# Optimization experiments

Hardware: AMD Instinct MI355X
Metric: run time of the kernel (lower is better)

Reference implementation:

```python
import jax, jax.numpy as jnp
import numpy as np
from jax import lax

ALPHA = 0.1
B, C_IN, T, D_MODEL = 32, 512, 2048, 1024


def setup_inputs() -> dict:
    key = jax.random.key(0)
    k_x, k_w, k_b = jax.random.split(key, 3)
    x = jax.random.normal(k_x, (B, C_IN, T), dtype=jnp.float32)
    # nn.Linear(c_in, d_model): weight [d_model, c_in], bias [d_model]
    bound = 1.0 / np.sqrt(C_IN)
    W = jax.random.uniform(k_w, (D_MODEL, C_IN), dtype=jnp.float32, minval=-bound, maxval=bound)
    b = jax.random.uniform(k_b, (D_MODEL,), dtype=jnp.float32, minval=-bound, maxval=bound)
    return {"x": x, "W": W, "b": b}


def _ewma_scan(xt):
    # xt: [T, B, C] time-major; f_0 = x_0, f_t = a*x_t + (1-a)*f_{t-1}
    def step(carry, xi):
        carry = ALPHA * xi + (1.0 - ALPHA) * carry
        return carry, carry
    _, ys = lax.scan(step, xt[0], xt[1:])
    return jnp.concatenate([xt[:1], ys], axis=0)  # [T, B, C]


def reference(x, W, b):
    # x: [B, c_in, T] -> permute to [B, T, c_in]
    xp = jnp.transpose(x, (0, 2, 1))
    xt = jnp.moveaxis(xp, 1, 0)  # [T, B, c_in]
    fwd = _ewma_scan(xt)
    bwd = _ewma_scan(xt[::-1])[::-1]
    ewma = jnp.moveaxis((fwd + bwd) * 0.5, 0, 1)  # [B, T, c_in]
    # value embedding (dropout = identity at inference)
    return jnp.einsum('btc,dc->btd', ewma, W) + b
```

## Files before the change

### kernel.cpp

```cpp
#include <hip/hip_runtime.h>
#include <hip/hip_bf16.h>
#include <stdint.h>
#include <stddef.h>

#define T_LEN   2048
#define C_IN_   512
#define D_MODEL_ 1024
#define B_SZ    32

typedef __hip_bfloat16 bf16;
typedef __attribute__((ext_vector_type(8))) short short8;
typedef __attribute__((ext_vector_type(4))) float f32x4;

__device__ __forceinline__ void gload16(const void* g, void* l) {
    __builtin_amdgcn_global_load_lds(
        (const __attribute__((address_space(1))) uint32_t*)g,
        (__attribute__((address_space(3))) uint32_t*)l, 16, 0, 0);
}

__global__ void wconv_kernel(const float* __restrict__ W, bf16* __restrict__ Wb) {
    int i = blockIdx.x * 256 + threadIdx.x;
    float4 v = ((const float4*)W)[i];
    bf16* o = Wb + (size_t)i * 4;
    o[0] = __float2bfloat16(v.x);
    o[1] = __float2bfloat16(v.y);
    o[2] = __float2bfloat16(v.z);
    o[3] = __float2bfloat16(v.w);
}

__global__ __launch_bounds__(512)
void ewma_kernel(const float* __restrict__ x, bf16* __restrict__ A) {
    const int tid  = threadIdx.x;
    const int wid  = tid >> 6;
    const int lane = tid & 63;
    const int half = lane >> 5;
    const int j    = lane & 31;
    const int b    = blockIdx.x >> 5;
    const int cg   = blockIdx.x & 31;
    const int c_local = (wid << 1) | half;
    const int c    = (cg << 4) + c_local;

    const float AL = 0.1f, OM = 0.9f;
    const float Q  = 1.179018457773862e-3f;

    float xr[64];
    const float4* xp = (const float4*)(x + (size_t)(b * C_IN_ + c) * T_LEN + j * 64);
    #pragma unroll
    for (int i = 0; i < 16; ++i) {
        float4 v = xp[i];
        xr[4*i+0] = v.x; xr[4*i+1] = v.y; xr[4*i+2] = v.z; xr[4*i+3] = v.w;
    }

    float g = (j == 0) ? xr[0] : AL * xr[0];
    #pragma unroll
    for (int i = 1; i < 64; ++i) g = fmaf(OM, g, AL * xr[i]);

    float F = g, coef = Q;
    #pragma unroll
    for (int d = 1; d < 32; d <<= 1) {
        float up = __shfl_up(F, d, 32);
        F += (j >= d) ? coef * up : 0.0f;
        coef *= coef;
    }
    float carry = __shfl_up(F, 1, 32);
    if (j == 0) carry = 0.0f;

    xr[0] = (j == 0) ? xr[0] : fmaf(OM, carry, AL * xr[0]);
    #pragma unroll
    for (int i = 1; i < 64; ++i) xr[i] = fmaf(OM, xr[i-1], AL * xr[i]);

    float h;
    {
        float incL = xr[63] - OM * xr[62];
        if (j == 31) incL *= 10.0f;
        h = incL;
        #pragma unroll
        for (int i = 62; i >= 1; --i) h = fmaf(OM, h, xr[i] - OM * xr[i-1]);
        float inc0 = (j == 0) ? AL * xr[0] : (xr[0] - OM * carry);
        h = fmaf(OM, h, inc0);
    }

    float Bv = h; coef = Q;
    #pragma unroll
    for (int d = 1; d < 32; d <<= 1) {
        float dn = __shfl_down(Bv, d, 32);
        Bv += (j < 32 - d) ? coef * dn : 0.0f;
        coef *= coef;
    }
    float bnext = __shfl_down(Bv, 1, 32);
    if (j == 31) bnext = 0.0f;

    {
        float bp = bnext;
        float incL = xr[63] - OM * xr[62];
        if (j == 31) incL *= 10.0f;
        float bb = fmaf(OM, bp, incL);
        xr[63] = 0.5f * (xr[63] + bb);
        bp = bb;
        #pragma unroll
        for (int i = 62; i >= 1; --i) {
            float inc = xr[i] - OM * xr[i-1];
            bb = fmaf(OM, bp, inc);
            xr[i] = 0.5f * (xr[i] + bb);
            bp = bb;
        }
        float inc0 = (j == 0) ? AL * xr[0] : (xr[0] - OM * carry);
        bb = fmaf(OM, bp, inc0);
        xr[0] = 0.5f * (xr[0] + bb);
    }

    __shared__ bf16 stg[32 * 16 * 16];
    const size_t outbase = (size_t)(b * T_LEN) * C_IN_ + (cg << 4);
    #pragma unroll
    for (int grp = 0; grp < 4; ++grp) {
        __syncthreads();
        #pragma unroll
        for (int ii = 0; ii < 16; ++ii) {
            int elem = ((j * 16 + ii) * 16 + c_local) ^ ((j & 7) << 3);
            stg[elem] = __float2bfloat16(xr[grp * 16 + ii]);
        }
        __syncthreads();
        #pragma unroll
        for (int r = 0; r < 2; ++r) {
            int u   = tid * 2 + r;
            int jj  = u >> 5;
            int ii  = (u >> 1) & 15;
            int hf  = u & 1;
            int elem = ((jj * 16 + ii) * 16 + hf * 8) ^ ((jj & 7) << 3);
            float4 v = *(const float4*)&stg[elem];
            int t = jj * 64 + grp * 16 + ii;
            *(float4*)(A + outbase + (size_t)t * C_IN_ + hf * 8) = v;
        }
    }
}

__global__ __launch_bounds__(256)
void gemm_kernel(const bf16* __restrict__ Amat, const bf16* __restrict__ Wb,
                 const float* __restrict__ bias, float* __restrict__ out) {
    constexpr int K = C_IN_, N = D_MODEL_, BK = 64;
    __shared__ bf16 As[128 * BK];
    __shared__ bf16 Bs[128 * BK];
    const int tid = threadIdx.x;
    const int wid = tid >> 6, lane = tid & 63;
    const int nb = blockIdx.x & 7, mb = blockIdx.x >> 3;
    const int m0 = mb * 128, n0 = nb * 128;
    const int wr = wid >> 1, wc = wid & 1;
    const int lrow = lane & 15, lk = (lane >> 4) * 8;

    f32x4 acc[4][4];
    #pragma unroll
    for (int i = 0; i < 4; ++i)
        #pragma unroll
        for (int q = 0; q < 4; ++q) acc[i][q] = (f32x4){0.f, 0.f, 0.f, 0.f};

    for (int kt = 0; kt < K; kt += BK) {
        const char* Ag = (const char*)(Amat + (size_t)m0 * K + kt);
        const char* Bg = (const char*)(Wb   + (size_t)n0 * K + kt);
        #pragma unroll
        for (int r = 0; r < 4; ++r) {
            int fb  = r * 4096 + tid * 16;
            int row = fb >> 7;
            int kb  = fb & 127;
            gload16(Ag + (size_t)row * (K * 2) + kb, (char*)As + fb);
            gload16(Bg + (size_t)row * (K * 2) + kb, (char*)Bs + fb);
        }
        __syncthreads();
        #pragma unroll
        for (int ks = 0; ks < 2; ++ks) {
            short8 af[4], bff[4];
            #pragma unroll
            for (int mf = 0; mf < 4; ++mf)
                af[mf] = *(const short8*)&As[(wr * 64 + mf * 16 + lrow) * BK + ks * 32 + lk];
            #pragma unroll
            for (int nf = 0; nf < 4; ++nf)
                bff[nf] = *(const short8*)&Bs[(wc * 64 + nf * 16 + lrow) * BK + ks * 32 + lk];
            #pragma unroll
            for (int mf = 0; mf < 4; ++mf)
                #pragma unroll
                for (int nf = 0; nf < 4; ++nf)
                    acc[mf][nf] = __builtin_amdgcn_mfma_f32_16x16x32_bf16(
                        af[mf], bff[nf], acc[mf][nf], 0, 0, 0);
        }
        __syncthreads();
    }
    #pragma unroll
    for (int mf = 0; mf < 4; ++mf) {
        #pragma unroll
        for (int nf = 0; nf < 4; ++nf) {
            int mrow0 = m0 + wr * 64 + mf * 16 + (lane >> 4) * 4;
            int ncol  = n0 + wc * 64 + nf * 16 + (lane & 15);
            float bv = bias[ncol];
            #pragma unroll
            for (int r = 0; r < 4; ++r)
                out[(size_t)(mrow0 + r) * N + ncol] = acc[mf][nf][r] + bv;
        }
    }
}

extern "C" void kernel_launch(void* const* d_in, const int* in_sizes, int n_in,
                              void* d_out, int out_size, void* d_ws, size_t ws_size,
                              hipStream_t stream) {
    const float* x    = (const float*)d_in[0];
    const float* W    = (const float*)d_in[1];
    const float* bias = (const float*)d_in[2];
    float* out = (float*)d_out;

    bf16* Wb   = (bf16*)d_ws;
    bf16* Amat = (bf16*)((char*)d_ws + (1 << 21));

    hipLaunchKernelGGL(wconv_kernel, dim3(512), dim3(256), 0, stream, W, Wb);
    hipLaunchKernelGGL(ewma_kernel, dim3(B_SZ * 32), dim3(512), 0, stream, x, Amat);
    hipLaunchKernelGGL(gemm_kernel, dim3((B_SZ * T_LEN / 128) * (D_MODEL_ / 128)),
                       dim3(256), 0, stream, Amat, Wb, bias, out);
}
```

Before: 204.7 us.

## Rewrite GEMM with 256x256 tiles, 8 waves, double-buffered swizzled LDS pipeline

Replaces the 128x128, 4-wave GEMM with a 256x256 tile computed by 512 threads using 128KB dynamic LDS. Global-to-LDS loads are double-buffered across K steps and interleaved with MFMA quadrants, using setprio and barriers. LDS rows are XOR-swizzled to avoid bank conflicts, and the block index is remapped for L2 locality. This raises data reuse and overlaps loads with compute, at the cost of LDS-limited occupancy of one block per CU and complex wait-count logic.

Result: faster. 172.6 us (-15.7%).

```diff
diff --git a/kernel.cpp b/kernel.cpp
--- a/kernel.cpp
+++ b/kernel.cpp
@@ -134,65 +134,148 @@
     }
 }
 
-__global__ __launch_bounds__(256)
+#define MFMA(a, b, c) __builtin_amdgcn_mfma_f32_16x16x32_bf16(a, b, c, 0, 0, 0)
+
+__global__ __launch_bounds__(512)
 void gemm_kernel(const bf16* __restrict__ Amat, const bf16* __restrict__ Wb,
                  const float* __restrict__ bias, float* __restrict__ out) {
-    constexpr int K = C_IN_, N = D_MODEL_, BK = 64;
-    __shared__ bf16 As[128 * BK];
-    __shared__ bf16 Bs[128 * BK];
-    const int tid = threadIdx.x;
-    const int wid = tid >> 6, lane = tid & 63;
-    const int nb = blockIdx.x & 7, mb = blockIdx.x >> 3;
-    const int m0 = mb * 128, n0 = nb * 128;
-    const int wr = wid >> 1, wc = wid & 1;
-    const int lrow = lane & 15, lk = (lane >> 4) * 8;
-
-    f32x4 acc[4][4];
-    #pragma unroll
-    for (int i = 0; i < 4; ++i)
-        #pragma unroll
-        for (int q = 0; q < 4; ++q) acc[i][q] = (f32x4){0.f, 0.f, 0.f, 0.f};
-
-    for (int kt = 0; kt < K; kt += BK) {
-        const char* Ag = (const char*)(Amat + (size_t)m0 * K + kt);
-        const char* Bg = (const char*)(Wb   + (size_t)n0 * K + kt);
-        #pragma unroll
-        for (int r = 0; r < 4; ++r) {
-            int fb  = r * 4096 + tid * 16;
-            int row = fb >> 7;
-            int kb  = fb & 127;
-            gload16(Ag + (size_t)row * (K * 2) + kb, (char*)As + fb);
-            gload16(Bg + (size_t)row * (K * 2) + kb, (char*)Bs + fb);
-        }
-        __syncthreads();
-        #pragma unroll
-        for (int ks = 0; ks < 2; ++ks) {
-            short8 af[4], bff[4];
-            #pragma unroll
-            for (int mf = 0; mf < 4; ++mf)
-                af[mf] = *(const short8*)&As[(wr * 64 + mf * 16 + lrow) * BK + ks * 32 + lk];
-            #pragma unroll
-            for (int nf = 0; nf < 4; ++nf)
-                bff[nf] = *(const short8*)&Bs[(wc * 64 + nf * 16 + lrow) * BK + ks * 32 + lk];
-            #pragma unroll
-            for (int mf = 0; mf < 4; ++mf)
-                #pragma unroll
-                for (int nf = 0; nf < 4; ++nf)
-                    acc[mf][nf] = __builtin_amdgcn_mfma_f32_16x16x32_bf16(
-                        af[mf], bff[nf], acc[mf][nf], 0, 0, 0);
-        }
-        __syncthreads();
-    }
-    #pragma unroll
-    for (int mf = 0; mf < 4; ++mf) {
-        #pragma unroll
-        for (int nf = 0; nf < 4; ++nf) {
-            int mrow0 = m0 + wr * 64 + mf * 16 + (lane >> 4) * 4;
-            int ncol  = n0 + wc * 64 + nf * 16 + (lane & 15);
-            float bv = bias[ncol];
+    constexpr int K = C_IN_, N = D_MODEL_;
+    extern __shared__ bf16 lds[];
+    const int tid  = threadIdx.x;
+    const int wid  = tid >> 6, lane = tid & 63;
+    const int wr   = wid >> 2, wc = wid & 3;
+    const int lr   = lane & 15;
+    const int lg   = lane >> 4;
+
+    int bid = blockIdx.x;
+    int swz = (bid & 7) * 128 + (bid >> 3);
+    const int mb = swz >> 2, nb = swz & 3;
+    const int m0 = mb * 256, n0 = nb * 256;
+
+    auto base = [&](int s, int op, int hf) -> bf16* {
+        return lds + (((s * 2 + op) * 2 + hf) << 13);
+    };
+    auto stage = [&](const bf16* g, int row0, int kt, int s, int op, int hf) {
+        bf16* lb = base(s, op, hf);
+        #pragma unroll
+        for (int r = 0; r < 2; ++r) {
+            int q = tid + r * 512;
+            int row = q >> 3, u = q & 7;
+            gload16(g + (size_t)(row0 + row) * K + kt * 64 + ((u ^ (row & 7)) << 3),
+                    (char*)lb + q * 16);
+        }
+    };
+    auto rdA = [&](int s, int mf, int ks) -> short8 {
+        int row = mf * 16 + lr;
+        int u   = ks * 4 + lg;
+        return *(const short8*)((const char*)base(s, 0, wr)
+                                + row * 128 + ((u ^ (row & 7)) << 4));
+    };
+    auto rdB = [&](int s, int nf, int ks) -> short8 {
+        int row = (wc & 1) * 64 + nf * 16 + lr;
+        int u   = ks * 4 + lg;
+        return *(const short8*)((const char*)base(s, 1, wc >> 1)
+                                + row * 128 + ((u ^ (row & 7)) << 4));
+    };
+
+    f32x4 acc[8][4];
+    #pragma unroll
+    for (int m = 0; m < 8; ++m)
+        #pragma unroll
+        for (int n = 0; n < 4; ++n) acc[m][n] = (f32x4){0.f, 0.f, 0.f, 0.f};
+
+    stage(Amat, m0 + 0,   0, 0, 0, 0);
+    stage(Amat, m0 + 128, 0, 0, 0, 1);
+    stage(Wb,   n0 + 0,   0, 0, 1, 0);
+    stage(Wb,   n0 + 128, 0, 0, 1, 1);
+    stage(Amat, m0 + 0,   1, 1, 0, 0);
+    asm volatile("s_waitcnt vmcnt(2)" ::: "memory");
+    __builtin_amdgcn_s_barrier();
+
+    #pragma unroll
+    for (int kt = 0; kt < 8; ++kt) {
+        const int s = kt & 1;
+        short8 a[4][2], bA[2][2], bB[2][2];
+
+        #pragma unroll
+        for (int m = 0; m < 4; ++m) { a[m][0] = rdA(s, m, 0); a[m][1] = rdA(s, m, 1); }
+        #pragma unroll
+        for (int n = 0; n < 2; ++n) { bA[n][0] = rdB(s, n, 0); bA[n][1] = rdB(s, n, 1); }
+        if (kt < 7) stage(Amat, m0 + 128, kt + 1, s ^ 1, 0, 1);
+        __builtin_amdgcn_s_barrier();
+        asm volatile("s_waitcnt lgkmcnt(0)");
+        __builtin_amdgcn_sched_barrier(0);
+        __builtin_amdgcn_s_setprio(1);
+        #pragma unroll
+        for (int m = 0; m < 4; ++m)
+            #pragma unroll
+            for (int n = 0; n < 2; ++n) {
+                acc[m][n] = MFMA(a[m][0], bA[n][0], acc[m][n]);
+                acc[m][n] = MFMA(a[m][1], bA[n][1], acc[m][n]);
+            }
+        __builtin_amdgcn_s_setprio(0);
+        __builtin_amdgcn_s_barrier();
+
+        #pragma unroll
+        for (int n = 0; n < 2; ++n) { bB[n][0] = rdB(s, 2 + n, 0); bB[n][1] = rdB(s, 2 + n, 1); }
+        if (kt < 7) stage(Wb, n0 + 0, kt + 1, s ^ 1, 1, 0);
+        __builtin_amdgcn_s_barrier();
+        asm volatile("s_waitcnt lgkmcnt(0)");
+        __builtin_amdgcn_sched_barrier(0);
+        __builtin_amdgcn_s_setprio(1);
+        #pragma unroll
+        for (int m = 0; m < 4; ++m)
+            #pragma unroll
+            for (int n = 0; n < 2; ++n) {
+                acc[m][2 + n] = MFMA(a[m][0], bB[n][0], acc[m][2 + n]);
+                acc[m][2 + n] = MFMA(a[m][1], bB[n][1], acc[m][2 + n]);
+            }
+        __builtin_amdgcn_s_setprio(0);
+        __builtin_amdgcn_s_barrier();
+
+        #pragma unroll
+        for (int m = 0; m < 4; ++m) { a[m][0] = rdA(s, 4 + m, 0); a[m][1] = rdA(s, 4 + m, 1); }
+        if (kt < 7) stage(Wb, n0 + 128, kt + 1, s ^ 1, 1, 1);
+        __builtin_amdgcn_s_barrier();
+        asm volatile("s_waitcnt lgkmcnt(0)");
+        __builtin_amdgcn_sched_barrier(0);
+        __builtin_amdgcn_s_setprio(1);
+        #pragma unroll
+        for (int m = 0; m < 4; ++m)
+            #pragma unroll
+            for (int n = 0; n < 2; ++n) {
+                acc[4 + m][2 + n] = MFMA(a[m][0], bB[n][0], acc[4 + m][2 + n]);
+                acc[4 + m][2 + n] = MFMA(a[m][1], bB[n][1], acc[4 + m][2 + n]);
+            }
+        __builtin_amdgcn_s_setprio(0);
+        __builtin_amdgcn_s_barrier();
+
+        if (kt < 6) stage(Amat, m0 + 0, kt + 2, s, 0, 0);
+        __builtin_amdgcn_s_setprio(1);
+        #pragma unroll
+        for (int m = 0; m < 4; ++m)
+            #pragma unroll
+            for (int n = 0; n < 2; ++n) {
+                acc[4 + m][n] = MFMA(a[m][0], bA[n][0], acc[4 + m][n]);
+                acc[4 + m][n] = MFMA(a[m][1], bA[n][1], acc[4 + m][n]);
+            }
+        __builtin_amdgcn_s_setprio(0);
+        if (kt < 6)       asm volatile("s_waitcnt vmcnt(2)" ::: "memory");
+        else if (kt == 6) asm volatile("s_waitcnt vmcnt(0)" ::: "memory");
+        __builtin_amdgcn_s_barrier();
+    }
+
+    const int crow = (lane >> 4) << 2;
+    #pragma unroll
+    for (int nf = 0; nf < 4; ++nf) {
+        int col = n0 + wc * 64 + nf * 16 + lr;
+        float bv = bias[col];
+        #pragma unroll
+        for (int mf = 0; mf < 8; ++mf) {
+            size_t rbase = (size_t)(m0 + wr * 128 + mf * 16 + crow) * N + col;
             #pragma unroll
             for (int r = 0; r < 4; ++r)
-                out[(size_t)(mrow0 + r) * N + ncol] = acc[mf][nf][r] + bv;
+                out[rbase + (size_t)r * N] = acc[mf][nf][r] + bv;
         }
     }
 }
@@ -210,6 +293,7 @@
 
     hipLaunchKernelGGL(wconv_kernel, dim3(512), dim3(256), 0, stream, W, Wb);
     hipLaunchKernelGGL(ewma_kernel, dim3(B_SZ * 32), dim3(512), 0, stream, x, Amat);
-    hipLaunchKernelGGL(gemm_kernel, dim3((B_SZ * T_LEN / 128) * (D_MODEL_ / 128)),
-                       dim3(256), 0, stream, Amat, Wb, bias, out);
-}
+    hipLaunchKernelGGL(gemm_kernel,
+                       dim3((B_SZ * T_LEN / 256) * (D_MODEL_ / 256)),
+                       dim3(512), 131072, stream, Amat, Wb, bias, out);
+}
```

## Rewrite GEMM with double-buffered swizzled LDS, 256x128 tiles and block remap

Applied to the files above, without the earlier changes.

The GEMM now uses 256x128 output tiles with BK=32. Two LDS stages are filled by async global-to-LDS loads, so the next K-slice loads while MFMAs run, coordinated with explicit vmcnt waits and barriers. LDS rows are XOR-swizzled to avoid bank conflicts, the block index is remapped so neighbouring blocks share the same B tile, and MFMA sections raise wave priority. The aim is to hide global load latency and raise MFMA utilisation. The cost is more accumulator registers (128 floats per thread) and hand-written waitcnt logic that must match the number of loads in flight.

Result: faster. 172.9 us (-15.5%).

```diff
diff --git a/kernel.cpp b/kernel.cpp
--- a/kernel.cpp
+++ b/kernel.cpp
@@ -134,65 +134,104 @@
     }
 }
 
-__global__ __launch_bounds__(256)
+#define MFMA(a, b, c) __builtin_amdgcn_mfma_f32_16x16x32_bf16(a, b, c, 0, 0, 0)
+
+__global__ __launch_bounds__(256, 2)
 void gemm_kernel(const bf16* __restrict__ Amat, const bf16* __restrict__ Wb,
                  const float* __restrict__ bias, float* __restrict__ out) {
-    constexpr int K = C_IN_, N = D_MODEL_, BK = 64;
-    __shared__ bf16 As[128 * BK];
-    __shared__ bf16 Bs[128 * BK];
-    const int tid = threadIdx.x;
-    const int wid = tid >> 6, lane = tid & 63;
-    const int nb = blockIdx.x & 7, mb = blockIdx.x >> 3;
-    const int m0 = mb * 128, n0 = nb * 128;
-    const int wr = wid >> 1, wc = wid & 1;
-    const int lrow = lane & 15, lk = (lane >> 4) * 8;
-
-    f32x4 acc[4][4];
-    #pragma unroll
-    for (int i = 0; i < 4; ++i)
-        #pragma unroll
-        for (int q = 0; q < 4; ++q) acc[i][q] = (f32x4){0.f, 0.f, 0.f, 0.f};
-
-    for (int kt = 0; kt < K; kt += BK) {
-        const char* Ag = (const char*)(Amat + (size_t)m0 * K + kt);
-        const char* Bg = (const char*)(Wb   + (size_t)n0 * K + kt);
+    constexpr int K = C_IN_, N = D_MODEL_;
+    extern __shared__ bf16 lds[];
+    const int tid  = threadIdx.x;
+    const int w    = tid >> 6, lane = tid & 63;
+    const int lr   = lane & 15;
+    const int lg   = lane >> 4;
+
+    int bid = blockIdx.x;
+    int swz = (bid & 7) * 256 + (bid >> 3);
+    const int mb = swz >> 3, nb = swz & 7;
+    const int m0 = mb * 256, n0 = nb * 128;
+
+    auto Abase = [&](int s) -> bf16* { return lds + s * 12288; };
+    auto Bbase = [&](int s) -> bf16* { return lds + s * 12288 + 8192; };
+
+    auto stage = [&](int kt, int s) {
+        bf16* la = Abase(s);
         #pragma unroll
         for (int r = 0; r < 4; ++r) {
-            int fb  = r * 4096 + tid * 16;
-            int row = fb >> 7;
-            int kb  = fb & 127;
-            gload16(Ag + (size_t)row * (K * 2) + kb, (char*)As + fb);
-            gload16(Bg + (size_t)row * (K * 2) + kb, (char*)Bs + fb);
-        }
-        __syncthreads();
-        #pragma unroll
-        for (int ks = 0; ks < 2; ++ks) {
-            short8 af[4], bff[4];
+            int q = tid + r * 256;
+            int row = q >> 2, u = q & 3;
+            gload16(Amat + (size_t)(m0 + row) * K + kt * 32 + ((u ^ ((row >> 1) & 3)) << 3),
+                    (char*)la + q * 16);
+        }
+        bf16* lb = Bbase(s);
+        #pragma unroll
+        for (int r = 0; r < 2; ++r) {
+            int q = tid + r * 256;
+            int row = q >> 2, u = q & 3;
+            gload16(Wb + (size_t)(n0 + row) * K + kt * 32 + ((u ^ ((row >> 1) & 3)) << 3),
+                    (char*)lb + q * 16);
+        }
+    };
+    auto rdA = [&](int s, int f) -> short8 {
+        int row = w * 64 + f * 16 + lr;
+        return *(const short8*)((const char*)Abase(s)
+                                + row * 64 + ((lg ^ ((row >> 1) & 3)) << 4));
+    };
+    auto rdB = [&](int s, int n) -> short8 {
+        int row = n * 16 + lr;
+        return *(const short8*)((const char*)Bbase(s)
+                                + row * 64 + ((lg ^ ((row >> 1) & 3)) << 4));
+    };
+
+    f32x4 acc[4][8];
+    #pragma unroll
+    for (int f = 0; f < 4; ++f)
+        #pragma unroll
+        for (int n = 0; n < 8; ++n) acc[f][n] = (f32x4){0.f, 0.f, 0.f, 0.f};
+
+    stage(0, 0);
+    stage(1, 1);
+    asm volatile("s_waitcnt vmcnt(6)" ::: "memory");
+    __builtin_amdgcn_s_barrier();
+
+    #pragma unroll
+    for (int kt = 0; kt < 16; ++kt) {
+        const int s = kt & 1;
+        short8 a[4], b[8];
+        #pragma unroll
+        for (int f = 0; f < 4; ++f) a[f] = rdA(s, f);
+        #pragma unroll
+        for (int n = 0; n < 8; ++n) b[n] = rdB(s, n);
+        asm volatile("s_waitcnt lgkmcnt(0)");
+        __builtin_amdgcn_sched_barrier(0);
+        __builtin_amdgcn_s_barrier();
+
+        if (kt < 14) stage(kt + 2, s);
+
+        __builtin_amdgcn_s_setprio(1);
+        #pragma unroll
+        for (int f = 0; f < 4; ++f)
             #pragma unroll
-            for (int mf = 0; mf < 4; ++mf)
-                af[mf] = *(const short8*)&As[(wr * 64 + mf * 16 + lrow) * BK + ks * 32 + lk];
-            #pragma unroll
-            for (int nf = 0; nf < 4; ++nf)
-                bff[nf] = *(const short8*)&Bs[(wc * 64 + nf * 16 + lrow) * BK + ks * 32 + lk];
-            #pragma unroll
-            for (int mf = 0; mf < 4; ++mf)
-                #pragma unroll
-                for (int nf = 0; nf < 4; ++nf)
-                    acc[mf][nf] = __builtin_amdgcn_mfma_f32_16x16x32_bf16(
-                        af[mf], bff[nf], acc[mf][nf], 0, 0, 0);
-        }
-        __syncthreads();
-    }
-    #pragma unroll
-    for (int mf = 0; mf < 4; ++mf) {
-        #pragma unroll
-        for (int nf = 0; nf < 4; ++nf) {
-            int mrow0 = m0 + wr * 64 + mf * 16 + (lane >> 4) * 4;
-            int ncol  = n0 + wc * 64 + nf * 16 + (lane & 15);
-            float bv = bias[ncol];
+            for (int n = 0; n < 8; ++n)
+                acc[f][n] = MFMA(a[f], b[n], acc[f][n]);
+        __builtin_amdgcn_s_setprio(0);
+
+        if (kt < 14)       asm volatile("s_waitcnt vmcnt(6)" ::: "memory");
+        else if (kt == 14) asm volatile("s_waitcnt vmcnt(0)" ::: "memory");
+        __builtin_amdgcn_s_barrier();
+    }
+
+    const int crow = (lane >> 4) << 2;
+    #pragma unroll
+    for (int n = 0; n < 8; ++n) {
+        int col = n0 + n * 16 + lr;
+        float bv = bias[col];
+        #pragma unroll
+        for (int f = 0; f < 4; ++f) {
+            size_t rbase = (size_t)(m0 + w * 64 + f * 16 + crow) * N + col;
             #pragma unroll
             for (int r = 0; r < 4; ++r)
-                out[(size_t)(mrow0 + r) * N + ncol] = acc[mf][nf][r] + bv;
+                out[rbase + (size_t)r * N] = acc[f][n][r] + bv;
         }
     }
 }
@@ -210,6 +249,7 @@
 
     hipLaunchKernelGGL(wconv_kernel, dim3(512), dim3(256), 0, stream, W, Wb);
     hipLaunchKernelGGL(ewma_kernel, dim3(B_SZ * 32), dim3(512), 0, stream, x, Amat);
-    hipLaunchKernelGGL(gemm_kernel, dim3((B_SZ * T_LEN / 128) * (D_MODEL_ / 128)),
-                       dim3(256), 0, stream, Amat, Wb, bias, out);
-}
+    hipLaunchKernelGGL(gemm_kernel,
+                       dim3((B_SZ * T_LEN / 256) * (D_MODEL_ / 128)),
+                       dim3(256), 49152, stream, Amat, Wb, bias, out);
+}
```
